# Kernel tuning notes

Measured on AMD Instinct MI355X. Metric: run time of the kernel, lower is better.

Reference implementation:

```python
import jax, jax.numpy as jnp
import numpy as np

# Module config (matches init_kwargs)
B, Cin, Cout = 2, 64, 64
D, H, W = 8, 48, 48
KD = KH = KW = 3
K = KD * KH * KW           # num_pts = 27
STRIDE, PAD, DIL = 1, 1, 1  # same-padded -> output spatial == input spatial


def setup_inputs() -> dict:
    key = jax.random.key(0)
    k1, k2, k3, k4, k5 = jax.random.split(key, 5)
    x = jax.random.normal(k1, (B, Cin, D, H, W), jnp.float32)
    # offset conv: original inits weight to zero; use small random so sampling is exercised
    conv_offset_w = jax.random.normal(k2, (3 * K, Cin, KD, KH, KW), jnp.float32) * 0.01
    # original bias init: uniform(-bound, bound), bound = (3+3+3)//6 = 1
    conv_offset_b = jax.random.uniform(k3, (3 * K,), jnp.float32, -1.0, 1.0)
    weight = jax.random.normal(k4, (Cout, Cin, K), jnp.float32) * (1.0 / np.sqrt(Cin * K))
    bias = jax.random.normal(k5, (Cout,), jnp.float32) * 0.01
    return dict(x=x, conv_offset_w=conv_offset_w, conv_offset_b=conv_offset_b,
                weight=weight, bias=bias)


def _trilinear_gather(x, pd, ph, pw):
    """x: [B,C,D,H,W]; pd/ph/pw: [B,K,Do,Ho,Wo] float sample coords.
    Returns [B,C,K,Do,Ho,Wo] trilinearly interpolated values (zeros out of bounds)."""
    Bn, C, Dd, Hh, Ww = x.shape
    x_flat = x.reshape(Bn, C, Dd * Hh * Ww)
    d0 = jnp.floor(pd); h0 = jnp.floor(ph); w0 = jnp.floor(pw)
    fd = pd - d0; fh = ph - h0; fw = pw - w0
    d0 = d0.astype(jnp.int32); h0 = h0.astype(jnp.int32); w0 = w0.astype(jnp.int32)
    sp = pd.shape  # [B,K,Do,Ho,Wo]
    acc = jnp.zeros((Bn, C) + sp[1:], x.dtype)
    gather = jax.vmap(lambda xf, ix: xf[:, ix])  # per-batch channelwise gather
    for cd in (0, 1):
        for ch in (0, 1):
            for cw in (0, 1):
                di = d0 + cd; hi = h0 + ch; wi = w0 + cw
                wgt = ((fd if cd else 1.0 - fd) *
                       (fh if ch else 1.0 - fh) *
                       (fw if cw else 1.0 - fw))
                valid = ((di >= 0) & (di < Dd) & (hi >= 0) & (hi < Hh) &
                         (wi >= 0) & (wi < Ww))
                idx = ((jnp.clip(di, 0, Dd - 1) * Hh + jnp.clip(hi, 0, Hh - 1)) * Ww
                       + jnp.clip(wi, 0, Ww - 1))
                g = gather(x_flat, idx.reshape(Bn, -1)).reshape((Bn, C) + sp[1:])
                acc = acc + g * (wgt * valid.astype(x.dtype))[:, None]
    return acc


def _forward(x, conv_offset_w, conv_offset_b, weight, bias):
    # offset conv (dim_mask = (1,1,1) -> identity multiply, omitted)
    offset = jax.lax.conv_general_dilated(
        x, conv_offset_w, window_strides=(STRIDE,) * 3,
        padding=[(PAD, PAD)] * 3,
        dimension_numbers=('NCDHW', 'OIDHW', 'NCDHW'))
    offset = offset + conv_offset_b[None, :, None, None, None]
    Bn = x.shape[0]
    Do, Ho, Wo = offset.shape[2], offset.shape[3], offset.shape[4]
    # channel layout (dg=1): [3, K] -> dim-major, point-minor (per dim_mask construction)
    off = offset.reshape(Bn, 3, K, Do, Ho, Wo)
    kd, kh, kw = [a.reshape(-1) for a in jnp.meshgrid(
        jnp.arange(KD), jnp.arange(KH), jnp.arange(KW), indexing='ij')]
    base_d = (jnp.arange(Do) * STRIDE - PAD)[None, :, None, None] + (kd * DIL)[:, None, None, None]
    base_h = (jnp.arange(Ho) * STRIDE - PAD)[None, None, :, None] + (kh * DIL)[:, None, None, None]
    base_w = (jnp.arange(Wo) * STRIDE - PAD)[None, None, None, :] + (kw * DIL)[:, None, None, None]
    pd = off[:, 0] + base_d[None].astype(off.dtype)  # [B,K,Do,Ho,Wo]
    ph = off[:, 1] + base_h[None].astype(off.dtype)
    pw = off[:, 2] + base_w[None].astype(off.dtype)
    vals = _trilinear_gather(x, pd, ph, pw)  # [B,Cin,K,Do,Ho,Wo]
    out = jnp.einsum('oik,bikdhw->bodhw', weight, vals)
    return out + bias[None, :, None, None, None]


def reference(x, conv_offset_w, conv_offset_b, weight, bias):
    return _forward(x, conv_offset_w, conv_offset_b, weight, bias)
```

## Files before the change

kernel.cpp:

```cpp
#include <hip/hip_runtime.h>
#include <hip/hip_fp16.h>

namespace {
constexpr int Bn = 2, Cin = 64, Cout = 64;
constexpr int Dd = 8, Hh = 48, Wd = 48;
constexpr int K = 27;
constexpr int SP = Dd * Hh * Wd;
constexpr int PLANE = Hh * Wd;
constexpr int NT32 = SP / 32;
constexpr int KC = 3;
constexpr int KPER = K / KC;
constexpr int CS = 2;
}

typedef __attribute__((ext_vector_type(8))) _Float16 half8;
typedef __attribute__((ext_vector_type(4))) float f32x4;

__device__ __forceinline__ unsigned short f2h(float f) {
  return __half_as_ushort(__float2half(f));
}
__device__ __forceinline__ __half2 u2h2(unsigned u) {
  return __builtin_bit_cast(__half2, u);
}
__device__ __forceinline__ unsigned h22u(__half2 h) {
  return __builtin_bit_cast(unsigned, h);
}

__global__ __launch_bounds__(256) void k_prep(const float* __restrict__ x,
                                              const float* __restrict__ w,
                                              const float* __restrict__ cw,
                                              unsigned short* __restrict__ xTh,
                                              unsigned short* __restrict__ wTb,
                                              unsigned short* __restrict__ wq) {
  int i = blockIdx.x * 256 + threadIdx.x;
  if (i < 2359296) {
    int c = i & 63;
    int rest = i >> 6;
    int p = rest % SP;
    int b = rest / SP;
    xTh[i] = f2h(x[(b * Cin + c) * SP + p]);
  } else if (i < 2359296 + 110592) {
    int i2 = i - 2359296;
    int j = i2 & 7, kg = (i2 >> 3) & 3, row = (i2 >> 5) & 15;
    int s = (i2 >> 9) & 1, mt = (i2 >> 10) & 3, k = i2 >> 12;
    int co = mt * 16 + row, cin = s * 32 + kg * 8 + j;
    wTb[i2] = f2h(w[((size_t)co * Cin + cin) * K + k]);
  } else {
    int i3 = i - 2469888;
    int j = i3 & 7, kg = (i3 >> 3) & 3, row = (i3 >> 5) & 15;
    int rest = i3 >> 9;
    int mt = rest % 6;
    int rest2 = rest / 6;
    int cs = rest2 & 1;
    int tap = rest2 >> 1;
    int ch = mt * 16 + row, cin = cs * 32 + kg * 8 + j;
    float v = (ch < 81) ? cw[((size_t)ch * 64 + cin) * 27 + tap] : 0.f;
    wq[i3] = f2h(v);
  }
}

__global__ __launch_bounds__(128) void k_offm3(const unsigned short* __restrict__ xTh,
                                               const unsigned short* __restrict__ wq,
                                               float* __restrict__ opart) {
  const int t = threadIdx.x;
  const int lane = t & 63;
  const int wv = t >> 6;
  const int bid = blockIdx.x;
  const int cs = bid / 1152;
  const int nb = bid - cs * 1152;
  const int n0 = nb * 32;
  const int b = n0 / SP;
  const int sp0 = n0 - b * SP;

  const int posl = lane & 15;
  const int quad = lane >> 4;
  const int q = sp0 + wv * 16 + posl;
  const int d = q / PLANE;
  const int rp = q - d * PLANE;
  const int h = rp / 48;
  const int w = rp - h * 48;
  const int grow = b * SP + q;

  const unsigned short* wbase = wq + cs * 3072 + posl * 32 + quad * 8;
  const int chof = cs * 32 + quad * 8;

  f32x4 acc[6];
#pragma unroll
  for (int mt = 0; mt < 6; ++mt) acc[mt] = f32x4{0.f, 0.f, 0.f, 0.f};

#pragma unroll
  for (int tap = 0; tap < 27; ++tap) {
    const int kd = tap / 9, kh = (tap % 9) / 3, kw = tap % 3;
    const int dd = d + kd - 1, hh = h + kh - 1, ww = w + kw - 1;
    const bool valid = ((unsigned)dd < 8u) & ((unsigned)hh < 48u) & ((unsigned)ww < 48u);
    const int delta = (kd - 1) * PLANE + (kh - 1) * 48 + (kw - 1);
    int row = grow + delta;
    row = min(max(row, 0), Bn * SP - 1);
    uint4 bu = *reinterpret_cast<const uint4*>(xTh + (size_t)row * 64 + chof);
    const unsigned m = valid ? 0xFFFFFFFFu : 0u;
    bu.x &= m; bu.y &= m; bu.z &= m; bu.w &= m;
    half8 bf = __builtin_bit_cast(half8, bu);
    const unsigned short* wt = wbase + tap * 6144;
#pragma unroll
    for (int mt = 0; mt < 6; ++mt) {
      half8 af = *reinterpret_cast<const half8*>(wt + mt * 512);
      acc[mt] = __builtin_amdgcn_mfma_f32_16x16x32_f16(af, bf, acc[mt], 0, 0, 0);
    }
  }

  const int colp = sp0 + wv * 16 + posl;
  float* pp = opart + (size_t)(cs * 2 + b) * 81 * SP;
#pragma unroll
  for (int mt = 0; mt < 6; ++mt) {
#pragma unroll
    for (int reg = 0; reg < 4; ++reg) {
      int ch = mt * 16 + quad * 4 + reg;
      if (ch < 81)
        pp[(size_t)ch * SP + colp] = acc[mt][reg];
    }
  }
}

__global__ __launch_bounds__(256) void k_offT(const float* __restrict__ opart,
                                              const float* __restrict__ cb,
                                              float* __restrict__ offT) {
  int i = blockIdx.x * 256 + threadIdx.x;
  int p4 = i % (SP / 4);
  int k = (i / (SP / 4)) % 27;
  int b = i / ((SP / 4) * 27);
  int kd = k / 9, kh = (k % 9) / 3, kw = k % 3;

  const float4* op4 = (const float4*)opart;
  float4 s[3];
#pragma unroll
  for (int dim = 0; dim < 3; ++dim) {
    int ch = dim * 27 + k;
    size_t base = (size_t)(b * 81 + ch) * (SP / 4) + p4;
    float4 v0 = op4[base];
    float4 v1 = op4[base + (size_t)2 * 81 * (SP / 4)];
    float bb = cb[ch];
    s[dim] = float4{v0.x + v1.x + bb, v0.y + v1.y + bb, v0.z + v1.z + bb,
                    v0.w + v1.w + bb};
  }
  float4* o4 = (float4*)offT + ((size_t)(b * 27 + k) * SP + p4 * 4);
#pragma unroll
  for (int e = 0; e < 4; ++e) {
    int p = p4 * 4 + e;
    int d = p / PLANE;
    int r = p - d * PLANE;
    int h = r / 48;
    int wp = r - h * 48;
    float se0 = (e == 0) ? s[0].x : (e == 1) ? s[0].y : (e == 2) ? s[0].z : s[0].w;
    float se1 = (e == 0) ? s[1].x : (e == 1) ? s[1].y : (e == 2) ? s[1].z : s[1].w;
    float se2 = (e == 0) ? s[2].x : (e == 1) ? s[2].y : (e == 2) ? s[2].z : s[2].w;
    o4[e] = float4{se0 + (float)(d + kd - 1), se1 + (float)(h + kh - 1),
                   se2 + (float)(wp + kw - 1), 0.f};
  }
}

__global__ __launch_bounds__(128, 8) void k_mainp(const unsigned short* __restrict__ xTh,
                                                  const float* __restrict__ offT,
                                                  const unsigned short* __restrict__ wTb,
                                                  float* __restrict__ part) {
  __shared__ __align__(16) unsigned scp[2][16 * 20];
  __shared__ __align__(16) unsigned short vals[2][16 * 72];

  const int t = threadIdx.x;
  const int lane = t & 63;
  const int wv = t >> 6;
  const int bid = blockIdx.x;
  const int kc = bid / 1152;
  const int j = bid - kc * 1152;
  const int tl = (j & 7) * 144 + (j >> 3);
  const int b = tl / NT32;
  const int tile = tl - b * NT32;
  const int p0 = tile * 32;

  const char* xb8 = (const char*)(xTh + (size_t)b * SP * 64);
  const float4* offTb = (const float4*)offT + (size_t)b * 27 * SP;

  const int posl = lane & 15;
  const int quad = lane >> 4;
  const int p = p0 + wv * 16 + posl;
  unsigned* myrow = &scp[wv][posl * 20];

  const int gpl0 = lane >> 3;
  const int gchg = lane & 7;

  f32x4 acc[4];
#pragma unroll
  for (int mt = 0; mt < 4; ++mt) acc[mt] = f32x4{0.f, 0.f, 0.f, 0.f};

  for (int kk = 0; kk < KPER; ++kk) {
    const int k = kc * KPER + kk;
    {
      float4 o = offTb[(size_t)k * SP + p];
      float df = floorf(o.x), hf = floorf(o.y), wf = floorf(o.z);
      float fd = o.x - df, fh = o.y - hf, fw = o.z - wf;
      int d0 = (int)df, h0 = (int)hf, w0i = (int)wf;
      unsigned pk[4];
#pragma unroll
      for (int cc = 0; cc < 2; ++cc) {
        int c = quad * 2 + cc;
        int cd = c >> 2, ch = (c >> 1) & 1, cwb = c & 1;
        int di = d0 + cd, hi = h0 + ch, wi = w0i + cwb;
        bool v = ((unsigned)di < 8u) && ((unsigned)hi < 48u) && ((unsigned)wi < 48u);
        float wg = (cd ? fd : 1.f - fd) * (ch ? fh : 1.f - fh) * (cwb ? fw : 1.f - fw);
        int dic = min(max(di, 0), 7), hic = min(max(hi, 0), 47), wic = min(max(wi, 0), 47);
        unsigned hs = (unsigned)f2h(v ? wg : 0.f);
        pk[cc * 2] = (unsigned)((dic * 48 + hic) * 48 + wic);
        pk[cc * 2 + 1] = hs | (hs << 16);
      }
      *reinterpret_cast<uint4*>(myrow + quad * 4) = uint4{pk[0], pk[1], pk[2], pk[3]};
    }
#pragma unroll
    for (int u = 0; u < 2; ++u) {
      const int pl = gpl0 + u * 8;
      const unsigned* sp = &scp[wv][pl * 20];
      const uint4 m0 = *reinterpret_cast<const uint4*>(sp + 0);
      const uint4 m1 = *reinterpret_cast<const uint4*>(sp + 4);
      const uint4 m2 = *reinterpret_cast<const uint4*>(sp + 8);
      const uint4 m3 = *reinterpret_cast<const uint4*>(sp + 12);
      const int cof = gchg << 4;
      uint4 q0 = *reinterpret_cast<const uint4*>(xb8 + (((size_t)m0.x << 7) + cof));
      uint4 q1 = *reinterpret_cast<const uint4*>(xb8 + (((size_t)m0.z << 7) + cof));
      uint4 q2 = *reinterpret_cast<const uint4*>(xb8 + (((size_t)m1.x << 7) + cof));
      uint4 q3 = *reinterpret_cast<const uint4*>(xb8 + (((size_t)m1.z << 7) + cof));
      uint4 q4 = *reinterpret_cast<const uint4*>(xb8 + (((size_t)m2.x << 7) + cof));
      uint4 q5 = *reinterpret_cast<const uint4*>(xb8 + (((size_t)m2.z << 7) + cof));
      uint4 q6 = *reinterpret_cast<const uint4*>(xb8 + (((size_t)m3.x << 7) + cof));
      uint4 q7 = *reinterpret_cast<const uint4*>(xb8 + (((size_t)m3.z << 7) + cof));
      __half2 a2[4];
#pragma unroll
      for (int e = 0; e < 4; ++e) a2[e] = u2h2(0u);
      __half2 w0 = u2h2(m0.y), w1 = u2h2(m0.w), w2 = u2h2(m1.y), w3 = u2h2(m1.w);
      __half2 w4 = u2h2(m2.y), w5 = u2h2(m2.w), w6 = u2h2(m3.y), w7 = u2h2(m3.w);
      a2[0] = __hfma2(u2h2(q0.x), w0, a2[0]); a2[1] = __hfma2(u2h2(q0.y), w0, a2[1]);
      a2[2] = __hfma2(u2h2(q0.z), w0, a2[2]); a2[3] = __hfma2(u2h2(q0.w), w0, a2[3]);
      a2[0] = __hfma2(u2h2(q1.x), w1, a2[0]); a2[1] = __hfma2(u2h2(q1.y), w1, a2[1]);
      a2[2] = __hfma2(u2h2(q1.z), w1, a2[2]); a2[3] = __hfma2(u2h2(q1.w), w1, a2[3]);
      a2[0] = __hfma2(u2h2(q2.x), w2, a2[0]); a2[1] = __hfma2(u2h2(q2.y), w2, a2[1]);
      a2[2] = __hfma2(u2h2(q2.z), w2, a2[2]); a2[3] = __hfma2(u2h2(q2.w), w2, a2[3]);
      a2[0] = __hfma2(u2h2(q3.x), w3, a2[0]); a2[1] = __hfma2(u2h2(q3.y), w3, a2[1]);
      a2[2] = __hfma2(u2h2(q3.z), w3, a2[2]); a2[3] = __hfma2(u2h2(q3.w), w3, a2[3]);
      a2[0] = __hfma2(u2h2(q4.x), w4, a2[0]); a2[1] = __hfma2(u2h2(q4.y), w4, a2[1]);
      a2[2] = __hfma2(u2h2(q4.z), w4, a2[2]); a2[3] = __hfma2(u2h2(q4.w), w4, a2[3]);
      a2[0] = __hfma2(u2h2(q5.x), w5, a2[0]); a2[1] = __hfma2(u2h2(q5.y), w5, a2[1]);
      a2[2] = __hfma2(u2h2(q5.z), w5, a2[2]); a2[3] = __hfma2(u2h2(q5.w), w5, a2[3]);
      a2[0] = __hfma2(u2h2(q6.x), w6, a2[0]); a2[1] = __hfma2(u2h2(q6.y), w6, a2[1]);
      a2[2] = __hfma2(u2h2(q6.z), w6, a2[2]); a2[3] = __hfma2(u2h2(q6.w), w6, a2[3]);
      a2[0] = __hfma2(u2h2(q7.x), w7, a2[0]); a2[1] = __hfma2(u2h2(q7.y), w7, a2[1]);
      a2[2] = __hfma2(u2h2(q7.z), w7, a2[2]); a2[3] = __hfma2(u2h2(q7.w), w7, a2[3]);
      *reinterpret_cast<uint4*>(&vals[wv][pl * 72 + gchg * 8]) =
          uint4{h22u(a2[0]), h22u(a2[1]), h22u(a2[2]), h22u(a2[3])};
    }
    {
      const unsigned short* wk = wTb + (size_t)k * 4096;
#pragma unroll
      for (int s = 0; s < 2; ++s) {
        half8 bfr = *reinterpret_cast<const half8*>(
            &vals[wv][posl * 72 + s * 32 + quad * 8]);
#pragma unroll
        for (int mt = 0; mt < 4; ++mt) {
          half8 afr = *reinterpret_cast<const half8*>(
              wk + mt * 1024 + s * 512 + posl * 32 + quad * 8);
          acc[mt] = __builtin_amdgcn_mfma_f32_16x16x32_f16(afr, bfr, acc[mt], 0, 0, 0);
        }
      }
    }
  }

  float* pp = part + ((size_t)(kc * 2 + b) * NT32 + tile) * 2048;
#pragma unroll
  for (int mt = 0; mt < 4; ++mt) {
#pragma unroll
    for (int reg = 0; reg < 4; ++reg) {
      int co = mt * 16 + quad * 4 + reg;
      pp[co * 32 + wv * 16 + posl] = acc[mt][reg];
    }
  }
}

__global__ __launch_bounds__(256) void k_red(const float* __restrict__ part,
                                             const float* __restrict__ bias,
                                             float* __restrict__ out) {
  int i = blockIdx.x * 256 + threadIdx.x;
  int p4 = i % (SP / 4);
  int co = (i / (SP / 4)) & 63;
  int b = i / ((SP / 4) * 64);
  int p = p4 * 4;
  int tile = p >> 5, pos = p & 31;
  size_t base = ((size_t)(b * NT32) + tile) * 2048 + co * 32 + pos;
  float4 s = *reinterpret_cast<const float4*>(&part[base]);
#pragma unroll
  for (int kc = 1; kc < KC; ++kc) {
    float4 v = *reinterpret_cast<const float4*>(
        &part[base + (size_t)kc * 2 * NT32 * 2048]);
    s.x += v.x; s.y += v.y; s.z += v.z; s.w += v.w;
  }
  float bb = bias[co];
  s.x += bb; s.y += bb; s.z += bb; s.w += bb;
  *reinterpret_cast<float4*>(&out[((size_t)(b * 64 + co)) * SP + p]) = s;
}

extern "C" void kernel_launch(void* const* d_in, const int* in_sizes, int n_in,
                              void* d_out, int out_size, void* d_ws, size_t ws_size,
                              hipStream_t stream) {
  const float* x = (const float*)d_in[0];
  const float* cw = (const float*)d_in[1];
  const float* cb = (const float*)d_in[2];
  const float* w = (const float*)d_in[3];
  const float* bias = (const float*)d_in[4];
  float* out = (float*)d_out;

  char* ws = (char*)d_ws;
  float* offT = (float*)ws;
  unsigned short* xTh = (unsigned short*)(ws + 15925248);
  unsigned short* wTb = (unsigned short*)(ws + 20643840);
  unsigned short* wq = (unsigned short*)(ws + 20865024);
  float* part = (float*)(ws + 21196800);
  float* opart = (float*)(ws + 49508352);

  hipLaunchKernelGGL(k_prep, dim3(10296), dim3(256), 0, stream, x, w, cw, xTh, wTb, wq);
  hipLaunchKernelGGL(k_offm3, dim3(CS * 1152), dim3(128), 0, stream, xTh, wq, opart);
  hipLaunchKernelGGL(k_offT, dim3(972), dim3(256), 0, stream, opart, cb, offT);
  hipLaunchKernelGGL(k_mainp, dim3(KC * 1152), dim3(128), 0, stream, xTh, offT, wTb, part);
  hipLaunchKernelGGL(k_red, dim3(2304), dim3(256), 0, stream, part, bias, out);
}
```

Before: 158.9 us.

## Store partial sums in fp16 and widen offset-conv blocks to 256 threads

```diff
diff --git a/kernel.cpp b/kernel.cpp
--- a/kernel.cpp
+++ b/kernel.cpp
@@ -59,16 +59,16 @@
   }
 }
 
-__global__ __launch_bounds__(128) void k_offm3(const unsigned short* __restrict__ xTh,
+__global__ __launch_bounds__(256) void k_offm3(const unsigned short* __restrict__ xTh,
                                                const unsigned short* __restrict__ wq,
-                                               float* __restrict__ opart) {
+                                               unsigned short* __restrict__ opart) {
   const int t = threadIdx.x;
   const int lane = t & 63;
   const int wv = t >> 6;
   const int bid = blockIdx.x;
-  const int cs = bid / 1152;
-  const int nb = bid - cs * 1152;
-  const int n0 = nb * 32;
+  const int cs = bid / 576;
+  const int nb = bid - cs * 576;
+  const int n0 = nb * 64;
   const int b = n0 / SP;
   const int sp0 = n0 - b * SP;
 
@@ -90,6 +90,7 @@
 
 #pragma unroll
   for (int tap = 0; tap < 27; ++tap) {
+    __builtin_amdgcn_s_barrier();
     const int kd = tap / 9, kh = (tap % 9) / 3, kw = tap % 3;
     const int dd = d + kd - 1, hh = h + kh - 1, ww = w + kw - 1;
     const bool valid = ((unsigned)dd < 8u) & ((unsigned)hh < 48u) & ((unsigned)ww < 48u);
@@ -109,19 +110,19 @@
   }
 
   const int colp = sp0 + wv * 16 + posl;
-  float* pp = opart + (size_t)(cs * 2 + b) * 81 * SP;
+  unsigned short* pp = opart + (size_t)(cs * 2 + b) * 81 * SP;
 #pragma unroll
   for (int mt = 0; mt < 6; ++mt) {
 #pragma unroll
     for (int reg = 0; reg < 4; ++reg) {
       int ch = mt * 16 + quad * 4 + reg;
       if (ch < 81)
-        pp[(size_t)ch * SP + colp] = acc[mt][reg];
-    }
-  }
-}
-
-__global__ __launch_bounds__(256) void k_offT(const float* __restrict__ opart,
+        pp[(size_t)ch * SP + colp] = f2h(acc[mt][reg]);
+    }
+  }
+}
+
+__global__ __launch_bounds__(256) void k_offT(const unsigned short* __restrict__ opart,
                                               const float* __restrict__ cb,
                                               float* __restrict__ offT) {
   int i = blockIdx.x * 256 + threadIdx.x;
@@ -130,17 +131,22 @@
   int b = i / ((SP / 4) * 27);
   int kd = k / 9, kh = (k % 9) / 3, kw = k % 3;
 
-  const float4* op4 = (const float4*)opart;
-  float4 s[3];
+  const __half2* op2 = (const __half2*)opart;
+  float s[3][4];
 #pragma unroll
   for (int dim = 0; dim < 3; ++dim) {
     int ch = dim * 27 + k;
-    size_t base = (size_t)(b * 81 + ch) * (SP / 4) + p4;
-    float4 v0 = op4[base];
-    float4 v1 = op4[base + (size_t)2 * 81 * (SP / 4)];
     float bb = cb[ch];
-    s[dim] = float4{v0.x + v1.x + bb, v0.y + v1.y + bb, v0.z + v1.z + bb,
-                    v0.w + v1.w + bb};
+    size_t e0 = (((size_t)(b * 81 + ch)) * SP + p4 * 4) >> 1;
+    size_t e1 = (((size_t)((2 + b) * 81 + ch)) * SP + p4 * 4) >> 1;
+    float2 a0 = __half22float2(op2[e0]);
+    float2 a1 = __half22float2(op2[e0 + 1]);
+    float2 c0 = __half22float2(op2[e1]);
+    float2 c1 = __half22float2(op2[e1 + 1]);
+    s[dim][0] = a0.x + c0.x + bb;
+    s[dim][1] = a0.y + c0.y + bb;
+    s[dim][2] = a1.x + c1.x + bb;
+    s[dim][3] = a1.y + c1.y + bb;
   }
   float4* o4 = (float4*)offT + ((size_t)(b * 27 + k) * SP + p4 * 4);
 #pragma unroll
@@ -150,18 +156,15 @@
     int r = p - d * PLANE;
     int h = r / 48;
     int wp = r - h * 48;
-    float se0 = (e == 0) ? s[0].x : (e == 1) ? s[0].y : (e == 2) ? s[0].z : s[0].w;
-    float se1 = (e == 0) ? s[1].x : (e == 1) ? s[1].y : (e == 2) ? s[1].z : s[1].w;
-    float se2 = (e == 0) ? s[2].x : (e == 1) ? s[2].y : (e == 2) ? s[2].z : s[2].w;
-    o4[e] = float4{se0 + (float)(d + kd - 1), se1 + (float)(h + kh - 1),
-                   se2 + (float)(wp + kw - 1), 0.f};
+    o4[e] = float4{s[0][e] + (float)(d + kd - 1), s[1][e] + (float)(h + kh - 1),
+                   s[2][e] + (float)(wp + kw - 1), 0.f};
   }
 }
 
 __global__ __launch_bounds__(128, 8) void k_mainp(const unsigned short* __restrict__ xTh,
                                                   const float* __restrict__ offT,
                                                   const unsigned short* __restrict__ wTb,
-                                                  float* __restrict__ part) {
+                                                  unsigned short* __restrict__ part) {
   __shared__ __align__(16) unsigned scp[2][16 * 20];
   __shared__ __align__(16) unsigned short vals[2][16 * 72];
 
@@ -270,18 +273,18 @@
     }
   }
 
-  float* pp = part + ((size_t)(kc * 2 + b) * NT32 + tile) * 2048;
+  unsigned short* pp = part + ((size_t)(kc * 2 + b) * NT32 + tile) * 2048;
 #pragma unroll
   for (int mt = 0; mt < 4; ++mt) {
 #pragma unroll
     for (int reg = 0; reg < 4; ++reg) {
       int co = mt * 16 + quad * 4 + reg;
-      pp[co * 32 + wv * 16 + posl] = acc[mt][reg];
-    }
-  }
-}
-
-__global__ __launch_bounds__(256) void k_red(const float* __restrict__ part,
+      pp[co * 32 + wv * 16 + posl] = f2h(acc[mt][reg]);
+    }
+  }
+}
+
+__global__ __launch_bounds__(256) void k_red(const unsigned short* __restrict__ part,
                                              const float* __restrict__ bias,
                                              float* __restrict__ out) {
   int i = blockIdx.x * 256 + threadIdx.x;
@@ -291,15 +294,16 @@
   int p = p4 * 4;
   int tile = p >> 5, pos = p & 31;
   size_t base = ((size_t)(b * NT32) + tile) * 2048 + co * 32 + pos;
-  float4 s = *reinterpret_cast<const float4*>(&part[base]);
-#pragma unroll
-  for (int kc = 1; kc < KC; ++kc) {
-    float4 v = *reinterpret_cast<const float4*>(
-        &part[base + (size_t)kc * 2 * NT32 * 2048]);
-    s.x += v.x; s.y += v.y; s.z += v.z; s.w += v.w;
-  }
+  const __half2* h2 = (const __half2*)part;
   float bb = bias[co];
-  s.x += bb; s.y += bb; s.z += bb; s.w += bb;
+  float4 s = float4{bb, bb, bb, bb};
+#pragma unroll
+  for (int kc = 0; kc < KC; ++kc) {
+    size_t e = (base + (size_t)kc * 2 * NT32 * 2048) >> 1;
+    float2 a = __half22float2(h2[e]);
+    float2 c = __half22float2(h2[e + 1]);
+    s.x += a.x; s.y += a.y; s.z += c.x; s.w += c.y;
+  }
   *reinterpret_cast<float4*>(&out[((size_t)(b * 64 + co)) * SP + p]) = s;
 }
 
@@ -318,11 +322,11 @@
   unsigned short* xTh = (unsigned short*)(ws + 15925248);
   unsigned short* wTb = (unsigned short*)(ws + 20643840);
   unsigned short* wq = (unsigned short*)(ws + 20865024);
-  float* part = (float*)(ws + 21196800);
-  float* opart = (float*)(ws + 49508352);
+  unsigned short* part = (unsigned short*)(ws + 21196800);
+  unsigned short* opart = (unsigned short*)(ws + 35352576);
 
   hipLaunchKernelGGL(k_prep, dim3(10296), dim3(256), 0, stream, x, w, cw, xTh, wTb, wq);
-  hipLaunchKernelGGL(k_offm3, dim3(CS * 1152), dim3(128), 0, stream, xTh, wq, opart);
+  hipLaunchKernelGGL(k_offm3, dim3(CS * 576), dim3(256), 0, stream, xTh, wq, opart);
   hipLaunchKernelGGL(k_offT, dim3(972), dim3(256), 0, stream, opart, cb, offT);
   hipLaunchKernelGGL(k_mainp, dim3(KC * 1152), dim3(128), 0, stream, xTh, offT, wTb, part);
   hipLaunchKernelGGL(k_red, dim3(2304), dim3(256), 0, stream, part, bias, out);
```

After: 162.2 us. 2.1% more time.
